# Performance work log

Hardware: AMD Instinct MI355X
Metric: run time of the kernel (lower is better)

The kernel has to match this reference:

```python
import jax, jax.numpy as jnp
import numpy as np

B, T, H = 16384, 1024, 32


def setup_inputs() -> dict:
    key = jax.random.key(0)
    ks = jax.random.split(key, 7)
    inv_sqrt_h = 1.0 / np.sqrt(H).astype(np.float32)
    return {
        "x": jax.random.normal(ks[0], (B, T), dtype=jnp.float32),
        "Wxh": jax.random.normal(ks[1], (1, H), dtype=jnp.float32),
        "b_xh": jax.random.normal(ks[2], (H,), dtype=jnp.float32) * 0.1,
        "Whh": jax.random.normal(ks[3], (H, H), dtype=jnp.float32) * inv_sqrt_h,
        "b_hh": jax.random.normal(ks[4], (H,), dtype=jnp.float32) * 0.1,
        "Wout": jax.random.normal(ks[5], (H, 1), dtype=jnp.float32) * inv_sqrt_h,
        "b_out": jax.random.normal(ks[6], (1,), dtype=jnp.float32) * 0.1,
    }


def reference(x, Wxh, b_xh, Whh, b_hh, Wout, b_out):
    # x: [B, T]. Each timestep feeds a scalar feature (in_dim=1).
    # h_{t} = tanh(h_{t-1} @ Whh + b_hh + x_t * Wxh + b_xh)
    h0 = jnp.zeros((x.shape[0], H), dtype=x.dtype)

    def step(h, xt):  # xt: [B]
        h_new = jnp.tanh(h @ Whh + b_hh + xt[:, None] * Wxh[0] + b_xh)
        return h_new, None

    hT, _ = jax.lax.scan(step, h0, x.T)  # scan over time: xs [T, B]
    return hT @ Wout + b_out  # [B, 1]
```

## Files before the change

### kernel.cpp

```cpp
#include <hip/hip_runtime.h>
#include <stdint.h>


typedef _Float16 half8  __attribute__((ext_vector_type(8)));
typedef float    f32x4  __attribute__((ext_vector_type(4)));
typedef uint32_t u32x4  __attribute__((ext_vector_type(4)));

constexpr int Tlen   = 1024;
constexpr int NTILES = 16384 / 16;

constexpr float KSC = 2.8853900817779268f;

__device__ __forceinline__ float sig_r(float argP) {
    float e = __builtin_amdgcn_exp2f(argP);
    return __builtin_amdgcn_rcpf(1.0f + e);
}

__device__ __forceinline__ uint32_t tanh_pack_pair(float rLo, float rHi,
                                                   float cm2, float c1) {
    uint32_t w;
    asm("v_fma_mixlo_f16 %0, %1, %2, %3" : "=v"(w) : "v"(rLo), "v"(cm2), "v"(c1));
    asm("v_fma_mixhi_f16 %0, %1, %2, %3" : "+v"(w) : "v"(rHi), "v"(cm2), "v"(c1));
    return w;
}

__device__ __forceinline__ void pl32swap(uint32_t& xv, uint32_t& yv) {
    asm("v_permlane32_swap_b32 %0, %1" : "+v"(xv), "+v"(yv));
}

__global__ __launch_bounds__(64, 1)
void rnn_scan_mfma(const float* __restrict__ x,
                   const float* __restrict__ Wxh,
                   const float* __restrict__ b_xh,
                   const float* __restrict__ Whh,
                   const float* __restrict__ b_hh,
                   const float* __restrict__ Wout,
                   const float* __restrict__ b_out,
                   float* __restrict__ out)
{
    const int  lane = threadIdx.x;
    const int  r16  = lane & 15;
    const int  G    = lane >> 4;
    const int  tile = blockIdx.x;

    const int mq   = r16 >> 2;
    const int mqp  = ((mq & 1) << 1) | (mq >> 1);
    const int col0 = 4 * mqp + (r16 & 3);

    half8 W1a, W1b;
    #pragma unroll
    for (int e = 0; e < 8; ++e) {
        int i = 8 * G + e;
        W1a[e] = (_Float16)(KSC * Whh[i * 32 + col0]);
        W1b[e] = (_Float16)(KSC * Whh[i * 32 + col0 + 16]);
    }

    const int gp = ((G & 1) << 1) | (G >> 1);
    const int jb = 4 * gp;
    float wx0[4], wx1[4], bb0[4], bb1[4], wo0[4], wo1[4];
    #pragma unroll
    for (int q = 0; q < 4; ++q) {
        int j0 = jb + q, j1 = j0 + 16;
        wx0[q] = KSC * Wxh[j0];
        bb0[q] = KSC * (b_hh[j0] + b_xh[j0]);
        wo0[q] = Wout[j0];
        wx1[q] = KSC * Wxh[j1];
        bb1[q] = KSC * (b_hh[j1] + b_xh[j1]);
        wo1[q] = Wout[j1];
    }
    const float bout = b_out[0];
    const float cm2 = -2.0f, c1 = 1.0f;

    const float* xrow = x + (size_t)(tile * 16 + r16) * Tlen;

    uint32_t b1w0 = 0, b1w1 = 0, b1w2 = 0, b1w3 = 0;
    float r0 = 0.5f, r1 = 0.5f, r2 = 0.5f, r3 = 0.5f;
    float r4 = 0.5f, r5 = 0.5f, r6 = 0.5f, r7 = 0.5f;

    auto step = [&](float xv) {
        f32x4 c0, c1v;
        #pragma unroll
        for (int q = 0; q < 4; ++q) {
            c0[q]  = __builtin_fmaf(xv, wx0[q], bb0[q]);
            c1v[q] = __builtin_fmaf(xv, wx1[q], bb1[q]);
        }

        u32x4 u1 = {b1w0, b1w1, b1w2, b1w3};
        half8 hb1 = __builtin_bit_cast(half8, u1);

        f32x4 a0 = __builtin_amdgcn_mfma_f32_16x16x32_f16(W1a, hb1, c0,  0, 0, 0);
        f32x4 a1 = __builtin_amdgcn_mfma_f32_16x16x32_f16(W1b, hb1, c1v, 0, 0, 0);

        r0 = sig_r(a0[0]);
        r1 = sig_r(a0[1]);
        r2 = sig_r(a0[2]);
        r3 = sig_r(a0[3]);
        r4 = sig_r(a1[0]);
        r5 = sig_r(a1[1]);
        r6 = sig_r(a1[2]);
        r7 = sig_r(a1[3]);

        uint32_t wA0 = tanh_pack_pair(r0, r1, cm2, c1);
        uint32_t wA1 = tanh_pack_pair(r2, r3, cm2, c1);
        uint32_t wB0 = tanh_pack_pair(r4, r5, cm2, c1);
        uint32_t wB1 = tanh_pack_pair(r6, r7, cm2, c1);
        pl32swap(wA0, wB0);  b1w0 = wA0;  b1w2 = wB0;
        pl32swap(wA1, wB1);  b1w1 = wA1;  b1w3 = wB1;
    };

    float4 xa = *(const float4*)&xrow[0];
    float4 xb = *(const float4*)&xrow[4];
    #pragma unroll 1
    for (int t8 = 0; t8 < Tlen / 8 - 1; ++t8) {
        float4 na = *(const float4*)&xrow[8 * t8 +  8];
        float4 nb = *(const float4*)&xrow[8 * t8 + 12];
        step(xa.x); step(xa.y); step(xa.z); step(xa.w);
        step(xb.x); step(xb.y); step(xb.z); step(xb.w);
        xa = na; xb = nb;
    }
    step(xa.x); step(xa.y); step(xa.z); step(xa.w);
    step(xb.x); step(xb.y); step(xb.z); step(xb.w);

    float t0 = __builtin_fmaf(cm2, r0, c1), t1 = __builtin_fmaf(cm2, r1, c1);
    float t2 = __builtin_fmaf(cm2, r2, c1), t3 = __builtin_fmaf(cm2, r3, c1);
    float t4 = __builtin_fmaf(cm2, r4, c1), t5 = __builtin_fmaf(cm2, r5, c1);
    float t6 = __builtin_fmaf(cm2, r6, c1), t7 = __builtin_fmaf(cm2, r7, c1);
    float v = t0 * wo0[0] + t1 * wo0[1] + t2 * wo0[2] + t3 * wo0[3]
            + t4 * wo1[0] + t5 * wo1[1] + t6 * wo1[2] + t7 * wo1[3];
    v += __shfl_xor(v, 16, 64);
    v += __shfl_xor(v, 32, 64);
    if (G == 0) out[tile * 16 + r16] = v + bout;
}

extern "C" void kernel_launch(void* const* d_in, const int* in_sizes, int n_in,
                              void* d_out, int out_size, void* d_ws, size_t ws_size,
                              hipStream_t stream) {
    const float* x     = (const float*)d_in[0];
    const float* Wxh   = (const float*)d_in[1];
    const float* b_xh  = (const float*)d_in[2];
    const float* Whh   = (const float*)d_in[3];
    const float* b_hh  = (const float*)d_in[4];
    const float* Wout  = (const float*)d_in[5];
    const float* b_out = (const float*)d_in[6];
    float* outp = (float*)d_out;

    rnn_scan_mfma<<<NTILES, 64, 0, stream>>>(x, Wxh, b_xh, Whh, b_hh, Wout,
                                             b_out, outp);
}
```

Baseline: 270.6 us.

## Split hidden state across two waves with LDS exchange per timestep

Each 16-row tile now uses two waves, and each wave computes half of the hidden units with a single MFMA and four sigmoids per step. The new hidden state is exchanged through double-buffered shared memory, with a block barrier every timestep, replacing the in-register permlane swap. The final output reduction now combines the two waves through shared memory. This shortens each wave's per-step dependency chain but adds an LDS write, a barrier and an LDS read to the serial critical path.

```diff
diff --git a/kernel.cpp b/kernel.cpp
--- a/kernel.cpp
+++ b/kernel.cpp
@@ -24,11 +24,7 @@
     return w;
 }
 
-__device__ __forceinline__ void pl32swap(uint32_t& xv, uint32_t& yv) {
-    asm("v_permlane32_swap_b32 %0, %1" : "+v"(xv), "+v"(yv));
-}
-
-__global__ __launch_bounds__(64, 1)
+__global__ __launch_bounds__(128, 1)
 void rnn_scan_mfma(const float* __restrict__ x,
                    const float* __restrict__ Wxh,
                    const float* __restrict__ b_xh,
@@ -38,74 +34,60 @@
                    const float* __restrict__ b_out,
                    float* __restrict__ out)
 {
-    const int  lane = threadIdx.x;
-    const int  r16  = lane & 15;
-    const int  G    = lane >> 4;
-    const int  tile = blockIdx.x;
+    __shared__ uint32_t hx[2][16][20];
+    __shared__ float    vred[2][16];
 
-    const int mq   = r16 >> 2;
-    const int mqp  = ((mq & 1) << 1) | (mq >> 1);
-    const int col0 = 4 * mqp + (r16 & 3);
+    const int tid  = threadIdx.x;
+    const int wv   = tid >> 6;
+    const int lane = tid & 63;
+    const int r16  = lane & 15;
+    const int G    = lane >> 4;
+    const int tile = blockIdx.x;
 
-    half8 W1a, W1b;
+    half8 W1;
     #pragma unroll
-    for (int e = 0; e < 8; ++e) {
-        int i = 8 * G + e;
-        W1a[e] = (_Float16)(KSC * Whh[i * 32 + col0]);
-        W1b[e] = (_Float16)(KSC * Whh[i * 32 + col0 + 16]);
-    }
+    for (int e = 0; e < 8; ++e)
+        W1[e] = (_Float16)(KSC * Whh[(8 * G + e) * 32 + 16 * wv + r16]);
 
-    const int gp = ((G & 1) << 1) | (G >> 1);
-    const int jb = 4 * gp;
-    float wx0[4], wx1[4], bb0[4], bb1[4], wo0[4], wo1[4];
+    float wx[4], bb[4], wo[4];
     #pragma unroll
     for (int q = 0; q < 4; ++q) {
-        int j0 = jb + q, j1 = j0 + 16;
-        wx0[q] = KSC * Wxh[j0];
-        bb0[q] = KSC * (b_hh[j0] + b_xh[j0]);
-        wo0[q] = Wout[j0];
-        wx1[q] = KSC * Wxh[j1];
-        bb1[q] = KSC * (b_hh[j1] + b_xh[j1]);
-        wo1[q] = Wout[j1];
+        int j = 16 * wv + 4 * G + q;
+        wx[q] = KSC * Wxh[j];
+        bb[q] = KSC * (b_hh[j] + b_xh[j]);
+        wo[q] = Wout[j];
     }
     const float bout = b_out[0];
     const float cm2 = -2.0f, c1 = 1.0f;
 
+    uint32_t* rdp[2] = { &hx[0][r16][4 * G],          &hx[1][r16][4 * G] };
+    uint32_t* wrp[2] = { &hx[0][r16][8 * wv + 2 * G], &hx[1][r16][8 * wv + 2 * G] };
+
+    *(uint2*)wrp[0] = make_uint2(0u, 0u);
+    __syncthreads();
+
     const float* xrow = x + (size_t)(tile * 16 + r16) * Tlen;
+    float r0 = 0.5f, r1 = 0.5f, r2 = 0.5f, r3 = 0.5f;
 
-    uint32_t b1w0 = 0, b1w1 = 0, b1w2 = 0, b1w3 = 0;
-    float r0 = 0.5f, r1 = 0.5f, r2 = 0.5f, r3 = 0.5f;
-    float r4 = 0.5f, r5 = 0.5f, r6 = 0.5f, r7 = 0.5f;
+    auto step = [&](float xv, const int p) {
+        f32x4 c;
+        #pragma unroll
+        for (int q = 0; q < 4; ++q) c[q] = __builtin_fmaf(xv, wx[q], bb[q]);
 
-    auto step = [&](float xv) {
-        f32x4 c0, c1v;
-        #pragma unroll
-        for (int q = 0; q < 4; ++q) {
-            c0[q]  = __builtin_fmaf(xv, wx0[q], bb0[q]);
-            c1v[q] = __builtin_fmaf(xv, wx1[q], bb1[q]);
-        }
+        u32x4 u  = *(const u32x4*)rdp[p];
+        half8 hb = __builtin_bit_cast(half8, u);
 
-        u32x4 u1 = {b1w0, b1w1, b1w2, b1w3};
-        half8 hb1 = __builtin_bit_cast(half8, u1);
+        f32x4 a = __builtin_amdgcn_mfma_f32_16x16x32_f16(W1, hb, c, 0, 0, 0);
 
-        f32x4 a0 = __builtin_amdgcn_mfma_f32_16x16x32_f16(W1a, hb1, c0,  0, 0, 0);
-        f32x4 a1 = __builtin_amdgcn_mfma_f32_16x16x32_f16(W1b, hb1, c1v, 0, 0, 0);
+        r0 = sig_r(a[0]);
+        r1 = sig_r(a[1]);
+        r2 = sig_r(a[2]);
+        r3 = sig_r(a[3]);
 
-        r0 = sig_r(a0[0]);
-        r1 = sig_r(a0[1]);
-        r2 = sig_r(a0[2]);
-        r3 = sig_r(a0[3]);
-        r4 = sig_r(a1[0]);
-        r5 = sig_r(a1[1]);
-        r6 = sig_r(a1[2]);
-        r7 = sig_r(a1[3]);
-
-        uint32_t wA0 = tanh_pack_pair(r0, r1, cm2, c1);
-        uint32_t wA1 = tanh_pack_pair(r2, r3, cm2, c1);
-        uint32_t wB0 = tanh_pack_pair(r4, r5, cm2, c1);
-        uint32_t wB1 = tanh_pack_pair(r6, r7, cm2, c1);
-        pl32swap(wA0, wB0);  b1w0 = wA0;  b1w2 = wB0;
-        pl32swap(wA1, wB1);  b1w1 = wA1;  b1w3 = wB1;
+        uint32_t wA = tanh_pack_pair(r0, r1, cm2, c1);
+        uint32_t wB = tanh_pack_pair(r2, r3, cm2, c1);
+        *(uint2*)wrp[p ^ 1] = make_uint2(wA, wB);
+        __syncthreads();
     };
 
     float4 xa = *(const float4*)&xrow[0];
@@ -114,22 +96,22 @@
     for (int t8 = 0; t8 < Tlen / 8 - 1; ++t8) {
         float4 na = *(const float4*)&xrow[8 * t8 +  8];
         float4 nb = *(const float4*)&xrow[8 * t8 + 12];
-        step(xa.x); step(xa.y); step(xa.z); step(xa.w);
-        step(xb.x); step(xb.y); step(xb.z); step(xb.w);
+        step(xa.x, 0); step(xa.y, 1); step(xa.z, 0); step(xa.w, 1);
+        step(xb.x, 0); step(xb.y, 1); step(xb.z, 0); step(xb.w, 1);
         xa = na; xb = nb;
     }
-    step(xa.x); step(xa.y); step(xa.z); step(xa.w);
-    step(xb.x); step(xb.y); step(xb.z); step(xb.w);
+    step(xa.x, 0); step(xa.y, 1); step(xa.z, 0); step(xa.w, 1);
+    step(xb.x, 0); step(xb.y, 1); step(xb.z, 0); step(xb.w, 1);
 
     float t0 = __builtin_fmaf(cm2, r0, c1), t1 = __builtin_fmaf(cm2, r1, c1);
     float t2 = __builtin_fmaf(cm2, r2, c1), t3 = __builtin_fmaf(cm2, r3, c1);
-    float t4 = __builtin_fmaf(cm2, r4, c1), t5 = __builtin_fmaf(cm2, r5, c1);
-    float t6 = __builtin_fmaf(cm2, r6, c1), t7 = __builtin_fmaf(cm2, r7, c1);
-    float v = t0 * wo0[0] + t1 * wo0[1] + t2 * wo0[2] + t3 * wo0[3]
-            + t4 * wo1[0] + t5 * wo1[1] + t6 * wo1[2] + t7 * wo1[3];
+    float v = t0 * wo[0] + t1 * wo[1] + t2 * wo[2] + t3 * wo[3];
     v += __shfl_xor(v, 16, 64);
     v += __shfl_xor(v, 32, 64);
-    if (G == 0) out[tile * 16 + r16] = v + bout;
+    if (lane < 16) vred[wv][r16] = v;
+    __syncthreads();
+    if (wv == 0 && lane < 16)
+        out[tile * 16 + r16] = vred[0][r16] + vred[1][r16] + bout;
 }
 
 extern "C" void kernel_launch(void* const* d_in, const int* in_sizes, int n_in,
@@ -144,6 +126,6 @@
     const float* b_out = (const float*)d_in[6];
     float* outp = (float*)d_out;
 
-    rnn_scan_mfma<<<NTILES, 64, 0, stream>>>(x, Wxh, b_xh, Whh, b_hh, Wout,
-                                             b_out, outp);
+    rnn_scan_mfma<<<NTILES, 128, 0, stream>>>(x, Wxh, b_xh, Whh, b_hh, Wout,
+                                              b_out, outp);
 }
```

After: 294.2 us. +8.7%, slower.
